# Optimization experiments

Hardware: AMD Instinct MI355X
Metric: run time of the kernel (lower is better)

The kernel has to match this reference:

```python
import jax, jax.numpy as jnp
import numpy as np

# ---- static config (mirrors HashEncoderHyFluid.__init__) ----
MIN_RES = np.array([16, 16, 16, 16], dtype=np.float64)
MAX_RES = np.array([256, 256, 256, 128], dtype=np.float64)
NUM_SCALES = 16
MAX_PARAMS = 2 ** 19
F = 2  # features_per_level
N_QUERIES = 1_000_000
PRIMES = np.array([1, 2654435761, 805459861, 3674653429], dtype=np.uint32)
# 16 corner offsets of the 4D hypercube, bit d of idx selects low/high along dim d
BITS = np.array([[(i >> d) & 1 for d in range(4)] for i in range(16)], dtype=np.int32)  # (16,4)


def build_config():
    b = np.exp((np.log(MAX_RES) - np.log(MIN_RES)) / (NUM_SCALES - 1))
    shapes, sizes, indicators, offsets = [], [], [], []
    total = 0
    for s in range(NUM_SCALES):
        res = np.ceil(MIN_RES * np.power(b, s)).astype(np.int64)
        raw = int(res[0] + 1) * int(res[1] + 1) * int(res[2] + 1) * int(res[3] + 1)
        p = raw if raw % 8 == 0 else ((raw + 7) // 8) * 8
        p = min(MAX_PARAMS, p)
        shapes.append(res)
        sizes.append(p)
        indicators.append(1 if raw <= p else 0)
        offsets.append(total)
        total += p * F
    return shapes, sizes, indicators, offsets, total


SHAPES, SIZES, INDICATORS, OFFSETS, TOTAL_HASH_SIZE = build_config()  # total = 15205344


def setup_inputs() -> dict:
    key = jax.random.key(0)
    k1, k2 = jax.random.split(key)
    xyzt = jax.random.uniform(k1, (N_QUERIES, 4), dtype=jnp.float32)  # coords in [0,1)
    hash_table = (jax.random.uniform(k2, (TOTAL_HASH_SIZE,), dtype=jnp.float32) * 2.0 - 1.0) * 0.001
    return {"xyzt": xyzt, "hash_table": hash_table}


def _encode_scale(xyzt, hash_table, res, size, indicator, offset):
    # xyzt: (N,4) in [0,1]; res: np int64 (4,)
    resf = jnp.asarray(res.astype(np.float32))
    pos = xyzt * resf                      # (N,4) grid-space position
    grid = jnp.floor(pos)
    frac = pos - grid                      # (N,4)
    grid = grid.astype(jnp.int32)
    corners = grid[:, None, :] + jnp.asarray(BITS)[None, :, :]          # (N,16,4)
    hi = jnp.asarray(BITS, jnp.float32)[None, :, :]                     # (1,16,4)
    w = jnp.prod(hi * frac[:, None, :] + (1.0 - hi) * (1.0 - frac[:, None, :]), axis=-1)  # (N,16)
    cu = corners.astype(jnp.uint32)
    if indicator == 1:
        # dense linear indexing: strides = cumprod(res+1), wrapping at uint32 like taichi
        strides = np.cumprod(np.concatenate([[1], (res + 1)[:3]])).astype(np.uint32)
        idx = jnp.sum(cu * jnp.asarray(strides), axis=-1)               # (N,16) uint32, wraps
    else:
        # xor hash with large primes
        h = cu[..., 0] * jnp.uint32(PRIMES[0])
        for d in range(1, 4):
            h = h ^ (cu[..., d] * jnp.uint32(PRIMES[d]))
        idx = h
    idx = (idx % jnp.uint32(size)).astype(jnp.int32)
    base = offset + idx * F                                             # (N,16)
    feats = hash_table[base[..., None] + jnp.arange(F)]                 # (N,16,F)
    return jnp.einsum("nc,ncf->nf", w, feats)                           # (N,F)


def reference(xyzt, hash_table):
    outs = []
    for s in range(NUM_SCALES):
        outs.append(_encode_scale(xyzt, hash_table, SHAPES[s], SIZES[s], INDICATORS[s], OFFSETS[s]))
    return jnp.concatenate(outs, axis=-1)  # (N, NUM_SCALES * F)
```

## Files before the change

kernel.cpp:

```cpp
#include <hip/hip_runtime.h>
#include <cstdint>
#include <cmath>


#define NSCALES 16
#define TPB 256
#define BINS 65536
#define QPB 128

struct Cfg {
  float    res[NSCALES][4];
  uint32_t key[NSCALES][4];
  uint32_t mask[NSCALES];
  int      offset[NSCALES];
  int      dense[NSCALES];
};

typedef float v4f __attribute__((ext_vector_type(4)));
typedef float v2f __attribute__((ext_vector_type(2)));

__device__ __forceinline__ uint32_t bucket_key(float x, float y, float z, float w)
{
  uint32_t bx = (uint32_t)(x * 16.f); bx = bx > 15u ? 15u : bx;
  uint32_t by = (uint32_t)(y * 16.f); by = by > 15u ? 15u : by;
  uint32_t bz = (uint32_t)(z * 16.f); bz = bz > 15u ? 15u : bz;
  uint32_t bt = (uint32_t)(w * 16.f); bt = bt > 15u ? 15u : bt;
  uint32_t k = 0;
#pragma unroll
  for (int b = 0; b < 4; ++b) {
    k |= ((bx >> b) & 1u) << (4 * b + 0);
    k |= ((by >> b) & 1u) << (4 * b + 1);
    k |= ((bz >> b) & 1u) << (4 * b + 2);
    k |= ((bt >> b) & 1u) << (4 * b + 3);
  }
  return k;
}

__global__ __launch_bounds__(TPB) void hist_kernel(
    const float* __restrict__ xyzt, uint32_t* __restrict__ hist, int N)
{
  const int i = blockIdx.x * TPB + threadIdx.x;
  if (i >= N) return;
  const v4f c = *(reinterpret_cast<const v4f*>(xyzt) + i);
  atomicAdd(&hist[bucket_key(c.x, c.y, c.z, c.w)], 1u);
}

__global__ __launch_bounds__(1024) void scan_kernel(
    const uint32_t* __restrict__ hist, uint32_t* __restrict__ cur)
{
  __shared__ uint32_t part[1024];
  const int t = threadIdx.x;
  const int base = t * (BINS / 1024);
  uint32_t s = 0;
  for (int j = 0; j < BINS / 1024; ++j) s += hist[base + j];
  part[t] = s;
  __syncthreads();
  for (int off = 1; off < 1024; off <<= 1) {
    uint32_t v = (t >= off) ? part[t - off] : 0u;
    __syncthreads();
    part[t] += v;
    __syncthreads();
  }
  uint32_t run = part[t] - s;
  for (int j = 0; j < BINS / 1024; ++j) {
    cur[base + j] = run;
    run += hist[base + j];
  }
}

__global__ __launch_bounds__(TPB) void scatter_kernel(
    const float* __restrict__ xyzt,
    uint32_t* __restrict__ cur,
    uint32_t* __restrict__ perm, float* __restrict__ c_sorted, int N)
{
  const int i = blockIdx.x * TPB + threadIdx.x;
  if (i >= N) return;
  const v4f c = *(reinterpret_cast<const v4f*>(xyzt) + i);
  const uint32_t k = bucket_key(c.x, c.y, c.z, c.w);
  const uint32_t pos = atomicAdd(&cur[k], 1u);
  perm[pos] = (uint32_t)i;
  *(reinterpret_cast<v4f*>(c_sorted) + pos) = c;
}

__global__ __launch_bounds__(TPB) void gather_kernel(
    const float*  __restrict__ coords,
    const float*  __restrict__ table,
    float2*       __restrict__ ws,
    int N, int s_base, Cfg cfg)
{
  const int s = (int)blockIdx.y + s_base;
  const int q = blockIdx.x * TPB + threadIdx.x;
  if (q >= N) return;
  const v4f c = *(reinterpret_cast<const v4f*>(coords) + q);

  const float rx = cfg.res[s][0], ry = cfg.res[s][1];
  const float rz = cfg.res[s][2], rw = cfg.res[s][3];
  const uint32_t K0 = cfg.key[s][0], K1 = cfg.key[s][1];
  const uint32_t K2 = cfg.key[s][2], K3 = cfg.key[s][3];

  const float px = c.x * rx, py = c.y * ry, pz = c.z * rz, pw = c.w * rw;
  const float gx = floorf(px), gy = floorf(py), gz = floorf(pz), gw = floorf(pw);
  const float fx = px - gx, fy = py - gy, fz = pz - gz, fw = pw - gw;
  const uint32_t ix = (uint32_t)(int)gx, iy = (uint32_t)(int)gy;
  const uint32_t iz = (uint32_t)(int)gz, iw = (uint32_t)(int)gw;

  const uint32_t x0 = ix * K0, x1 = x0 + K0;
  const uint32_t y0 = iy * K1, y1 = y0 + K1;
  const uint32_t z0 = iz * K2, z1 = z0 + K2;
  const uint32_t u0 = iw * K3, u1 = u0 + K3;

  const float wx0 = 1.f - fx, wy0 = 1.f - fy, wz0 = 1.f - fz, ww0 = 1.f - fw;
  const float wA[4] = { wx0 * wy0, fx * wy0, wx0 * fy, fx * fy };
  const float wB[4] = { wz0 * ww0, fz * ww0, wz0 * fw, fz * fw };

  const float*  tbf = table + cfg.offset[s];
  const float2* __restrict__ tb  = reinterpret_cast<const float2*>(tbf);
  const float4* __restrict__ tb4 = reinterpret_cast<const float4*>(tbf);

  float a0 = 0.f, a1 = 0.f;
  if (cfg.dense[s]) {
    const uint32_t hA[4] = { x0 + y0, x1 + y0, x0 + y1, x1 + y1 };
    const uint32_t hB[4] = { z0 + u0, z1 + u0, z0 + u1, z1 + u1 };
#pragma unroll
    for (int i = 0; i < 16; ++i) {
      const uint32_t idx = hA[i & 3] + hB[i >> 2];
      const float2 v = tb[idx];
      const float w = wA[i & 3] * wB[i >> 2];
      a0 = fmaf(w, v.x, a0);
      a1 = fmaf(w, v.y, a1);
    }
  } else {
    const uint32_t msk = cfg.mask[s];
    if ((ix & 1u) == 0u) {
      const uint32_t yv[2] = { y0, y1 };
      const uint32_t zw[4] = { z0 ^ u0, z1 ^ u0, z0 ^ u1, z1 ^ u1 };
#pragma unroll
      for (int j = 0; j < 8; ++j) {
        const int jy = j & 1, jz = j >> 1;
        const uint32_t p  = (x0 ^ yv[jy] ^ zw[jz]) & msk;
        const uint32_t e  = p & ~1u;
        const uint32_t sel = p & 1u;
        const float4 v = tb4[e >> 1];
        const float wlo = wA[2 * jy]     * wB[jz];
        const float whi = wA[2 * jy + 1] * wB[jz];
        const float l0 = sel ? v.z : v.x, l1 = sel ? v.w : v.y;
        const float h0 = sel ? v.x : v.z, h1 = sel ? v.y : v.w;
        a0 = fmaf(wlo, l0, fmaf(whi, h0, a0));
        a1 = fmaf(wlo, l1, fmaf(whi, h1, a1));
      }
    } else {
      const uint32_t hA[4] = { x0 ^ y0, x1 ^ y0, x0 ^ y1, x1 ^ y1 };
      const uint32_t hB[4] = { z0 ^ u0, z1 ^ u0, z0 ^ u1, z1 ^ u1 };
#pragma unroll
      for (int i = 0; i < 16; ++i) {
        const uint32_t idx = (hA[i & 3] ^ hB[i >> 2]) & msk;
        const float2 v = tb[idx];
        const float w = wA[i & 3] * wB[i >> 2];
        a0 = fmaf(w, v.x, a0);
        a1 = fmaf(w, v.y, a1);
      }
    }
  }
  v2f val = { a0, a1 };
  __builtin_nontemporal_store(val, (v2f*)&ws[(size_t)s * N + q]);
}

__global__ __launch_bounds__(TPB) void transpose_perm(
    const float2*   __restrict__ ws,
    const uint32_t* __restrict__ perm,
    float*          __restrict__ out,
    int N)
{
  __shared__ float2 st[NSCALES][QPB + 1];
  const int t  = threadIdx.x;
  const int q0 = blockIdx.x * QPB;
#pragma unroll
  for (int i = 0; i < (NSCALES * QPB) / TPB; ++i) {
    const int idx = i * TPB + t;
    const int sc  = idx >> 7;
    const int qi  = idx & (QPB - 1);
    const int q   = q0 + qi;
    const v2f tmp = __builtin_nontemporal_load(
        reinterpret_cast<const v2f*>(&ws[(size_t)sc * N + (q < N ? q : N - 1)]));
    st[sc][qi] = make_float2(tmp.x, tmp.y);
  }
  __syncthreads();
#pragma unroll
  for (int i = 0; i < (QPB * 8) / TPB; ++i) {
    const int g  = i * TPB + t;
    const int qi = g >> 3;
    const int h  = g & 7;
    const int q  = q0 + qi;
    if (q < N) {
      const float2 a = st[2 * h][qi];
      const float2 b = st[2 * h + 1][qi];
      const uint32_t pq = perm[q];
      v4f val = { a.x, a.y, b.x, b.y };
      __builtin_nontemporal_store(val, (v4f*)(out + (size_t)pq * 32 + h * 4));
    }
  }
}

__global__ __launch_bounds__(TPB) void transpose_kernel(
    const float2* __restrict__ ws,
    float*        __restrict__ out,
    int N)
{
  __shared__ float2 st[NSCALES][TPB + 1];
  const int t  = threadIdx.x;
  const int q  = blockIdx.x * TPB + t;
  const int ql = q < N ? q : N - 1;
#pragma unroll
  for (int s = 0; s < NSCALES; ++s)
    st[s][t] = ws[(size_t)s * N + ql];
  __syncthreads();
  const int base = blockIdx.x * (TPB * 2 * NSCALES);
#pragma unroll
  for (int it = 0; it < 8; ++it) {
    const int G  = it * 1024 + t * 4;
    const int qi = G >> 5;
    const int s0 = (G & 31) >> 1;
    if (blockIdx.x * TPB + qi < N) {
      const float2 a = st[s0][qi];
      const float2 b = st[s0 + 1][qi];
      v4f val = { a.x, a.y, b.x, b.y };
      __builtin_nontemporal_store(val, (v4f*)(out + base + G));
    }
  }
}

__global__ __launch_bounds__(TPB) void hashenc_fused(
    const float4* __restrict__ xyzt,
    const float*  __restrict__ table,
    float*        __restrict__ out,
    int N, Cfg cfg)
{
  __shared__ float2 st[NSCALES][TPB + 1];
  const int t  = threadIdx.x;
  const int q  = blockIdx.x * TPB + t;
  const int ql = q < N ? q : N - 1;
  const float4 c = xyzt[ql];
#pragma unroll 1
  for (int s = 0; s < NSCALES; ++s) {
    const float rx = cfg.res[s][0], ry = cfg.res[s][1];
    const float rz = cfg.res[s][2], rw = cfg.res[s][3];
    const uint32_t K0 = cfg.key[s][0], K1 = cfg.key[s][1];
    const uint32_t K2 = cfg.key[s][2], K3 = cfg.key[s][3];
    const float px = c.x * rx, py = c.y * ry, pz = c.z * rz, pw = c.w * rw;
    const float gx = floorf(px), gy = floorf(py), gz = floorf(pz), gw = floorf(pw);
    const float fx = px - gx, fy = py - gy, fz = pz - gz, fw = pw - gw;
    const uint32_t ix = (uint32_t)(int)gx, iy = (uint32_t)(int)gy;
    const uint32_t iz = (uint32_t)(int)gz, iw = (uint32_t)(int)gw;
    const uint32_t x0 = ix * K0, x1 = x0 + K0;
    const uint32_t y0 = iy * K1, y1 = y0 + K1;
    const uint32_t z0 = iz * K2, z1 = z0 + K2;
    const uint32_t u0 = iw * K3, u1 = u0 + K3;
    const float wx0 = 1.f - fx, wy0 = 1.f - fy, wz0 = 1.f - fz, ww0 = 1.f - fw;
    const float wA[4] = { wx0 * wy0, fx * wy0, wx0 * fy, fx * fy };
    const float wB[4] = { wz0 * ww0, fz * ww0, wz0 * fw, fz * fw };
    const float2* __restrict__ tb =
        reinterpret_cast<const float2*>(table + cfg.offset[s]);
    float a0 = 0.f, a1 = 0.f;
    if (cfg.dense[s]) {
      const uint32_t hA[4] = { x0 + y0, x1 + y0, x0 + y1, x1 + y1 };
      const uint32_t hB[4] = { z0 + u0, z1 + u0, z0 + u1, z1 + u1 };
#pragma unroll
      for (int i = 0; i < 16; ++i) {
        const uint32_t idx = hA[i & 3] + hB[i >> 2];
        const float2 v = tb[idx];
        const float w = wA[i & 3] * wB[i >> 2];
        a0 = fmaf(w, v.x, a0); a1 = fmaf(w, v.y, a1);
      }
    } else {
      const uint32_t msk = cfg.mask[s];
      const uint32_t hA[4] = { x0 ^ y0, x1 ^ y0, x0 ^ y1, x1 ^ y1 };
      const uint32_t hB[4] = { z0 ^ u0, z1 ^ u0, z0 ^ u1, z1 ^ u1 };
#pragma unroll
      for (int i = 0; i < 16; ++i) {
        const uint32_t idx = (hA[i & 3] ^ hB[i >> 2]) & msk;
        const float2 v = tb[idx];
        const float w = wA[i & 3] * wB[i >> 2];
        a0 = fmaf(w, v.x, a0); a1 = fmaf(w, v.y, a1);
      }
    }
    st[s][t] = make_float2(a0, a1);
  }
  __syncthreads();
  const int base = blockIdx.x * (TPB * 2 * NSCALES);
#pragma unroll
  for (int it = 0; it < 8; ++it) {
    const int G  = it * 1024 + t * 4;
    const int qi = G >> 5;
    const int s0 = (G & 31) >> 1;
    if (blockIdx.x * TPB + qi < N) {
      const float2 a = st[s0][qi];
      const float2 b = st[s0 + 1][qi];
      v4f val = { a.x, a.y, b.x, b.y };
      __builtin_nontemporal_store(val, (v4f*)(out + base + G));
    }
  }
}

static void build_cfg(Cfg& cfg)
{
  const double minr[4] = { 16.0, 16.0, 16.0, 16.0 };
  const double maxr[4] = { 256.0, 256.0, 256.0, 128.0 };
  const uint32_t primes[4] = { 1u, 2654435761u, 805459861u, 3674653429u };

  double b[4];
  for (int d = 0; d < 4; ++d)
    b[d] = ::exp((::log(maxr[d]) - ::log(minr[d])) / (double)(NSCALES - 1));

  long long total = 0;
  for (int s = 0; s < NSCALES; ++s) {
    long long res[4];
    for (int d = 0; d < 4; ++d)
      res[d] = (long long)::ceil(minr[d] * ::pow(b[d], (double)s));

    const long long raw =
        (res[0] + 1) * (res[1] + 1) * (res[2] + 1) * (res[3] + 1);
    long long p = (raw % 8 == 0) ? raw : ((raw + 7) / 8) * 8;
    if (p > 524288) p = 524288;
    const int ind = (raw <= p) ? 1 : 0;

    for (int d = 0; d < 4; ++d) cfg.res[s][d] = (float)res[d];
    if (ind) {
      cfg.key[s][0] = 1u;
      cfg.key[s][1] = (uint32_t)(res[0] + 1);
      cfg.key[s][2] = (uint32_t)((res[0] + 1) * (res[1] + 1));
      cfg.key[s][3] = (uint32_t)((res[0] + 1) * (res[1] + 1) * (res[2] + 1));
    } else {
      for (int d = 0; d < 4; ++d) cfg.key[s][d] = primes[d];
    }
    cfg.mask[s]   = (uint32_t)(p - 1);
    cfg.offset[s] = (int)total;
    cfg.dense[s]  = ind;
    total += p * 2;
  }
}

static inline size_t align_up(size_t v, size_t a) { return (v + a - 1) & ~(a - 1); }

extern "C" void kernel_launch(void* const* d_in, const int* in_sizes, int n_in,
                              void* d_out, int out_size, void* d_ws, size_t ws_size,
                              hipStream_t stream)
{
  const float* xyzt  = (const float*)d_in[0];
  const float* table = (const float*)d_in[1];
  float*       out   = (float*)d_out;
  const int N = in_sizes[0] / 4;

  Cfg cfg;
  build_cfg(cfg);

  const int qblocks = (N + TPB - 1) / TPB;

  size_t off = 0;
  const size_t perm_off = off;             off = align_up(off + (size_t)N * 4, 256);
  const size_t hist_off = off;             off = align_up(off + (size_t)BINS * 4, 256);
  const size_t cur_off  = off;             off = align_up(off + (size_t)BINS * 4, 256);
  const size_t cs_off   = align_up(off, 16);  off = cs_off + (size_t)N * 16;
  const size_t ws_off   = align_up(off, 16);
  const size_t need_sorted = ws_off + (size_t)N * NSCALES * sizeof(float2);
  const size_t need_plain  = (size_t)N * NSCALES * sizeof(float2);

  char* wsb = (char*)d_ws;

  if (ws_size >= need_sorted) {
    uint32_t* perm = (uint32_t*)(wsb + perm_off);
    uint32_t* hist = (uint32_t*)(wsb + hist_off);
    uint32_t* cur  = (uint32_t*)(wsb + cur_off);
    float*    csrt = (float*)(wsb + cs_off);
    float2*   ws   = (float2*)(wsb + ws_off);

    hipMemsetAsync(hist, 0, (size_t)BINS * 4, stream);
    hipLaunchKernelGGL(hist_kernel, dim3(qblocks), dim3(TPB), 0, stream,
                       xyzt, hist, N);
    hipLaunchKernelGGL(scan_kernel, dim3(1), dim3(1024), 0, stream, hist, cur);
    hipLaunchKernelGGL(scatter_kernel, dim3(qblocks), dim3(TPB), 0, stream,
                       xyzt, cur, perm, csrt, N);
    hipLaunchKernelGGL(gather_kernel, dim3(qblocks, NSCALES), dim3(TPB), 0,
                       stream, csrt, table, ws, N, 0, cfg);
    const int tblocks = (N + QPB - 1) / QPB;
    hipLaunchKernelGGL(transpose_perm, dim3(tblocks), dim3(TPB), 0, stream,
                       ws, perm, out, N);
  } else if (ws_size >= need_plain) {
    float2* ws = (float2*)d_ws;
    hipLaunchKernelGGL(gather_kernel, dim3(qblocks, NSCALES), dim3(TPB), 0,
                       stream, xyzt, table, ws, N, 0, cfg);
    hipLaunchKernelGGL(transpose_kernel, dim3(qblocks), dim3(TPB), 0,
                       stream, ws, out, N);
  } else {
    hipLaunchKernelGGL(hashenc_fused, dim3(qblocks), dim3(TPB), 0,
                       stream, (const float4*)xyzt, table, out, N, cfg);
  }
}
```

Measured before the change: 808.9 us.

## Fuse per-scale gather and permuted transpose into one kernel over sorted queries

Replaces the separate gather kernel (grid over queries × scales, writing an intermediate scale-major workspace) and the transpose_perm kernel with a single fused kernel. Each thread loads its query through the permutation, loops over all 16 scales, stages results in shared memory in two halves, and writes them straight to the output in original order. The scatter kernel no longer writes sorted coordinates, and the large intermediate buffer is dropped. The trade-off is less parallelism, since the grid is now per query instead of per query-scale pair. Each thread also runs a serial 16-scale loop with more registers, which can reduce how well latency is hidden on the random table gathers.

```diff
diff --git a/kernel.cpp b/kernel.cpp
--- a/kernel.cpp
+++ b/kernel.cpp
@@ -71,7 +71,7 @@
 __global__ __launch_bounds__(TPB) void scatter_kernel(
     const float* __restrict__ xyzt,
     uint32_t* __restrict__ cur,
-    uint32_t* __restrict__ perm, float* __restrict__ c_sorted, int N)
+    uint32_t* __restrict__ perm, int N)
 {
   const int i = blockIdx.x * TPB + threadIdx.x;
   if (i >= N) return;
@@ -79,7 +79,117 @@
   const uint32_t k = bucket_key(c.x, c.y, c.z, c.w);
   const uint32_t pos = atomicAdd(&cur[k], 1u);
   perm[pos] = (uint32_t)i;
-  *(reinterpret_cast<v4f*>(c_sorted) + pos) = c;
+}
+
+__global__ __launch_bounds__(TPB) void gather_fused(
+    const float*    __restrict__ xyzt,
+    const float*    __restrict__ table,
+    const uint32_t* __restrict__ perm,
+    float*          __restrict__ out,
+    int N, Cfg cfg)
+{
+  __shared__ float2   st[8][TPB + 1];
+  __shared__ uint32_t pql[TPB];
+  const int t  = threadIdx.x;
+  const int q  = blockIdx.x * TPB + t;
+  const int ql = q < N ? q : N - 1;
+  const uint32_t pq = perm[ql];
+  pql[t] = pq;
+  const v4f c = *(reinterpret_cast<const v4f*>(xyzt) + pq);
+
+#pragma unroll
+  for (int half = 0; half < 2; ++half) {
+#pragma unroll 1
+    for (int si = 0; si < 8; ++si) {
+      const int s = half * 8 + si;
+      const float rx = cfg.res[s][0], ry = cfg.res[s][1];
+      const float rz = cfg.res[s][2], rw = cfg.res[s][3];
+      const uint32_t K0 = cfg.key[s][0], K1 = cfg.key[s][1];
+      const uint32_t K2 = cfg.key[s][2], K3 = cfg.key[s][3];
+
+      const float px = c.x * rx, py = c.y * ry, pz = c.z * rz, pw = c.w * rw;
+      const float gx = floorf(px), gy = floorf(py);
+      const float gz = floorf(pz), gw = floorf(pw);
+      const float fx = px - gx, fy = py - gy, fz = pz - gz, fw = pw - gw;
+      const uint32_t ix = (uint32_t)(int)gx, iy = (uint32_t)(int)gy;
+      const uint32_t iz = (uint32_t)(int)gz, iw = (uint32_t)(int)gw;
+
+      const uint32_t x0 = ix * K0, x1 = x0 + K0;
+      const uint32_t y0 = iy * K1, y1 = y0 + K1;
+      const uint32_t z0 = iz * K2, z1 = z0 + K2;
+      const uint32_t u0 = iw * K3, u1 = u0 + K3;
+
+      const float wx0 = 1.f - fx, wy0 = 1.f - fy;
+      const float wz0 = 1.f - fz, ww0 = 1.f - fw;
+      const float wA[4] = { wx0 * wy0, fx * wy0, wx0 * fy, fx * fy };
+      const float wB[4] = { wz0 * ww0, fz * ww0, wz0 * fw, fz * fw };
+
+      const float*  tbf = table + cfg.offset[s];
+      const float2* __restrict__ tb  = reinterpret_cast<const float2*>(tbf);
+      const float4* __restrict__ tb4 = reinterpret_cast<const float4*>(tbf);
+
+      float a0 = 0.f, a1 = 0.f;
+      if (cfg.dense[s]) {
+        const uint32_t hA[4] = { x0 + y0, x1 + y0, x0 + y1, x1 + y1 };
+        const uint32_t hB[4] = { z0 + u0, z1 + u0, z0 + u1, z1 + u1 };
+#pragma unroll
+        for (int i = 0; i < 16; ++i) {
+          const uint32_t idx = hA[i & 3] + hB[i >> 2];
+          const float2 v = tb[idx];
+          const float w = wA[i & 3] * wB[i >> 2];
+          a0 = fmaf(w, v.x, a0);
+          a1 = fmaf(w, v.y, a1);
+        }
+      } else {
+        const uint32_t msk = cfg.mask[s];
+        if ((ix & 1u) == 0u) {
+          const uint32_t yv[2] = { y0, y1 };
+          const uint32_t zw[4] = { z0 ^ u0, z1 ^ u0, z0 ^ u1, z1 ^ u1 };
+#pragma unroll
+          for (int j = 0; j < 8; ++j) {
+            const int jy = j & 1, jz = j >> 1;
+            const uint32_t p  = (x0 ^ yv[jy] ^ zw[jz]) & msk;
+            const uint32_t e  = p & ~1u;
+            const uint32_t sel = p & 1u;
+            const float4 v = tb4[e >> 1];
+            const float wlo = wA[2 * jy]     * wB[jz];
+            const float whi = wA[2 * jy + 1] * wB[jz];
+            const float l0 = sel ? v.z : v.x, l1 = sel ? v.w : v.y;
+            const float h0 = sel ? v.x : v.z, h1 = sel ? v.y : v.w;
+            a0 = fmaf(wlo, l0, fmaf(whi, h0, a0));
+            a1 = fmaf(wlo, l1, fmaf(whi, h1, a1));
+          }
+        } else {
+          const uint32_t hA[4] = { x0 ^ y0, x1 ^ y0, x0 ^ y1, x1 ^ y1 };
+          const uint32_t hB[4] = { z0 ^ u0, z1 ^ u0, z0 ^ u1, z1 ^ u1 };
+#pragma unroll
+          for (int i = 0; i < 16; ++i) {
+            const uint32_t idx = (hA[i & 3] ^ hB[i >> 2]) & msk;
+            const float2 v = tb[idx];
+            const float w = wA[i & 3] * wB[i >> 2];
+            a0 = fmaf(w, v.x, a0);
+            a1 = fmaf(w, v.y, a1);
+          }
+        }
+      }
+      st[si][t] = make_float2(a0, a1);
+    }
+    __syncthreads();
+#pragma unroll
+    for (int i = 0; i < 4; ++i) {
+      const int g  = i * TPB + t;
+      const int qi = g >> 2;
+      const int h  = g & 3;
+      if (blockIdx.x * TPB + qi < N) {
+        const float2 a = st[2 * h][qi];
+        const float2 b = st[2 * h + 1][qi];
+        v4f val = { a.x, a.y, b.x, b.y };
+        __builtin_nontemporal_store(
+            val, (v4f*)(out + (size_t)pql[qi] * 32 + half * 16 + h * 4));
+      }
+    }
+    __syncthreads();
+  }
 }
 
 __global__ __launch_bounds__(TPB) void gather_kernel(
@@ -163,42 +273,6 @@
   }
   v2f val = { a0, a1 };
   __builtin_nontemporal_store(val, (v2f*)&ws[(size_t)s * N + q]);
-}
-
-__global__ __launch_bounds__(TPB) void transpose_perm(
-    const float2*   __restrict__ ws,
-    const uint32_t* __restrict__ perm,
-    float*          __restrict__ out,
-    int N)
-{
-  __shared__ float2 st[NSCALES][QPB + 1];
-  const int t  = threadIdx.x;
-  const int q0 = blockIdx.x * QPB;
-#pragma unroll
-  for (int i = 0; i < (NSCALES * QPB) / TPB; ++i) {
-    const int idx = i * TPB + t;
-    const int sc  = idx >> 7;
-    const int qi  = idx & (QPB - 1);
-    const int q   = q0 + qi;
-    const v2f tmp = __builtin_nontemporal_load(
-        reinterpret_cast<const v2f*>(&ws[(size_t)sc * N + (q < N ? q : N - 1)]));
-    st[sc][qi] = make_float2(tmp.x, tmp.y);
-  }
-  __syncthreads();
-#pragma unroll
-  for (int i = 0; i < (QPB * 8) / TPB; ++i) {
-    const int g  = i * TPB + t;
-    const int qi = g >> 3;
-    const int h  = g & 7;
-    const int q  = q0 + qi;
-    if (q < N) {
-      const float2 a = st[2 * h][qi];
-      const float2 b = st[2 * h + 1][qi];
-      const uint32_t pq = perm[q];
-      v4f val = { a.x, a.y, b.x, b.y };
-      __builtin_nontemporal_store(val, (v4f*)(out + (size_t)pq * 32 + h * 4));
-    }
-  }
 }
 
 __global__ __launch_bounds__(TPB) void transpose_kernel(
@@ -359,9 +433,7 @@
   const size_t perm_off = off;             off = align_up(off + (size_t)N * 4, 256);
   const size_t hist_off = off;             off = align_up(off + (size_t)BINS * 4, 256);
   const size_t cur_off  = off;             off = align_up(off + (size_t)BINS * 4, 256);
-  const size_t cs_off   = align_up(off, 16);  off = cs_off + (size_t)N * 16;
-  const size_t ws_off   = align_up(off, 16);
-  const size_t need_sorted = ws_off + (size_t)N * NSCALES * sizeof(float2);
+  const size_t need_sorted = off;
   const size_t need_plain  = (size_t)N * NSCALES * sizeof(float2);
 
   char* wsb = (char*)d_ws;
@@ -370,20 +442,15 @@
     uint32_t* perm = (uint32_t*)(wsb + perm_off);
     uint32_t* hist = (uint32_t*)(wsb + hist_off);
     uint32_t* cur  = (uint32_t*)(wsb + cur_off);
-    float*    csrt = (float*)(wsb + cs_off);
-    float2*   ws   = (float2*)(wsb + ws_off);
 
     hipMemsetAsync(hist, 0, (size_t)BINS * 4, stream);
     hipLaunchKernelGGL(hist_kernel, dim3(qblocks), dim3(TPB), 0, stream,
                        xyzt, hist, N);
     hipLaunchKernelGGL(scan_kernel, dim3(1), dim3(1024), 0, stream, hist, cur);
     hipLaunchKernelGGL(scatter_kernel, dim3(qblocks), dim3(TPB), 0, stream,
-                       xyzt, cur, perm, csrt, N);
-    hipLaunchKernelGGL(gather_kernel, dim3(qblocks, NSCALES), dim3(TPB), 0,
-                       stream, csrt, table, ws, N, 0, cfg);
-    const int tblocks = (N + QPB - 1) / QPB;
-    hipLaunchKernelGGL(transpose_perm, dim3(tblocks), dim3(TPB), 0, stream,
-                       ws, perm, out, N);
+                       xyzt, cur, perm, N);
+    hipLaunchKernelGGL(gather_fused, dim3(qblocks), dim3(TPB), 0, stream,
+                       xyzt, table, perm, out, N, cfg);
   } else if (ws_size >= need_plain) {
     float2* ws = (float2*)d_ws;
     hipLaunchKernelGGL(gather_kernel, dim3(qblocks, NSCALES), dim3(TPB), 0,
```

New measurement: 1.130 ms. 39.7% more time.
